# Performance work log

Hardware: AMD Instinct MI355X
Metric: run time of the kernel (lower is better)

The kernel has to match this reference:

```python
import jax, jax.numpy as jnp
import numpy as np

B = 4_194_304
N_LAYERS = 2


def setup_inputs() -> dict:
    key = jax.random.key(0)
    k1, k2 = jax.random.split(key)
    x = jax.random.normal(k1, (B, 2), dtype=jnp.float32)
    q_weights = 0.01 * jax.random.normal(k2, (N_LAYERS, 2), dtype=jnp.float32)
    return {"x": x, "q_weights": q_weights}


def _apply_rx(state, theta, qubit):
    """Apply RX(theta) to `qubit` of a batched 2-qubit state [B,2,2].
    RX(t) = [[cos(t/2), -i sin(t/2)], [-i sin(t/2), cos(t/2)]].
    theta: [B] (per-sample) or scalar (shared weight)."""
    b = state.shape[0]
    theta = jnp.broadcast_to(theta, (b,))
    c = jnp.cos(0.5 * theta)[:, None].astype(state.dtype)
    s = (-1j * jnp.sin(0.5 * theta))[:, None].astype(state.dtype)
    if qubit == 0:
        a0, a1 = state[:, 0, :], state[:, 1, :]
        return jnp.stack([c * a0 + s * a1, s * a0 + c * a1], axis=1)
    else:
        a0, a1 = state[:, :, 0], state[:, :, 1]
        return jnp.stack([c * a0 + s * a1, s * a0 + c * a1], axis=2)


def _cnot01(state):
    # control = qubit0, target = qubit1: swap target amps where control == 1
    return jnp.stack([state[:, 0, :], state[:, 1, ::-1]], axis=1)


def reference(x, q_weights):
    b = x.shape[0]
    # |00> initial state, batched: [B, 2, 2] (axes = qubit0, qubit1)
    state = jnp.zeros((b, 2, 2), dtype=jnp.complex64).at[:, 0, 0].set(1.0)
    # AngleEmbedding (default rotation = RX) with per-sample angles
    state = _apply_rx(state, x[:, 0], 0)
    state = _apply_rx(state, x[:, 1], 1)
    # BasicEntanglerLayers: per layer RX on each wire, then single CNOT(0,1)
    for l in range(q_weights.shape[0]):
        state = _apply_rx(state, q_weights[l, 0], 0)
        state = _apply_rx(state, q_weights[l, 1], 1)
        state = _cnot01(state)
    # <Z_0> = P(qubit0=0) - P(qubit0=1)
    probs = jnp.real(state * jnp.conj(state))
    expz0 = jnp.sum(probs[:, 0, :], axis=-1) - jnp.sum(probs[:, 1, :], axis=-1)
    return (0.5 * (expz0 + 1.0)).astype(jnp.float32).reshape(-1, 1)
```

## Files before the change

kernel.cpp:

```cpp
#include <hip/hip_runtime.h>
#include <math.h>

#define N_LAYERS 2

__device__ __forceinline__ void rx_pair(float2& a, float2& b, float c, float s) {
    float2 na = make_float2(fmaf(c, a.x,  s * b.y), fmaf(c, a.y, -s * b.x));
    float2 nb = make_float2(fmaf(s, a.y,  c * b.x), fmaf(-s, a.x, c * b.y));
    a = na; b = nb;
}

__global__ void qnet_precompute_K(const float* __restrict__ w, float* __restrict__ K) {
    if (threadIdx.x != 0 || blockIdx.x != 0) return;

    float2 U[4][4];
    for (int j = 0; j < 4; ++j)
        for (int r = 0; r < 4; ++r)
            U[j][r] = make_float2(j == r ? 1.f : 0.f, 0.f);

    for (int l = 0; l < N_LAYERS; ++l) {
        float t0 = 0.5f * w[2 * l + 0];
        float t1 = 0.5f * w[2 * l + 1];
        float c0 = cosf(t0), s0 = sinf(t0);
        float c1 = cosf(t1), s1 = sinf(t1);
        for (int j = 0; j < 4; ++j) {
            rx_pair(U[j][0], U[j][2], c0, s0);
            rx_pair(U[j][1], U[j][3], c0, s0);
            rx_pair(U[j][0], U[j][1], c1, s1);
            rx_pair(U[j][2], U[j][3], c1, s1);
            float2 tmp = U[j][2]; U[j][2] = U[j][3]; U[j][3] = tmp;
        }
    }

    float Mre[4][4], Mim[4][4];
    for (int j = 0; j < 4; ++j)
        for (int k = 0; k < 4; ++k) {
            float re = 0.f, im = 0.f;
            for (int m = 0; m < 2; ++m) {
                re += U[j][m].x * U[k][m].x + U[j][m].y * U[k][m].y;
                im += U[j][m].x * U[k][m].y - U[j][m].y * U[k][m].x;
            }
            Mre[j][k] = re; Mim[j][k] = im;
        }

    float N00 = Mre[0][0], N11 = Mre[1][1], N22 = Mre[2][2], N33 = Mre[3][3];
    float N01 = Mim[0][1];
    float N23 = Mim[2][3];
    float N02 = Mim[0][2];
    float N13 = Mim[1][3];
    float N03 = -Mre[0][3];
    float N12 = Mre[1][2];

    K[0] = 0.25f * (N00 + N11 + N22 + N33);
    K[1] = 0.25f * (N00 - N11 + N22 - N33);
    K[2] = 0.50f * (N01 + N23);
    K[3] = 0.25f * (N00 + N11 - N22 - N33);
    K[4] = 0.25f * (N00 - N11 - N22 + N33);
    K[5] = 0.50f * (N01 - N23);
    K[6] = 0.50f * (N02 + N13);
    K[7] = 0.50f * (N02 - N13);
    K[8] = 0.50f * (N03 + N12);
}

__device__ __forceinline__ float qnet_eval1(float x0, float x1,
                                            float k0, float k1, float k2,
                                            float k3, float k4, float k5,
                                            float k6, float k7, float k8) {
    float X0 = __cosf(x0), S0 = __sinf(x0);
    float X1 = __cosf(x1), S1 = __sinf(x1);
    float t0 = fmaf(k2, S1, fmaf(k1, X1, k0));
    float t1 = fmaf(k5, S1, fmaf(k4, X1, k3));
    float t2 = fmaf(k8, S1, fmaf(k7, X1, k6));
    return fmaf(S0, t2, fmaf(X0, t1, t0));
}

__global__ __launch_bounds__(256) void qnet_eval_kernel(
    const float4* __restrict__ x, const float* __restrict__ K,
    float2* __restrict__ out, int n2) {
    int i = blockIdx.x * blockDim.x + threadIdx.x;
    float k0 = K[0], k1 = K[1], k2 = K[2];
    float k3 = K[3], k4 = K[4], k5 = K[5];
    float k6 = K[6], k7 = K[7], k8 = K[8];
    if (i >= n2) return;
    float4 xv = x[i];
    float r0 = qnet_eval1(xv.x, xv.y, k0, k1, k2, k3, k4, k5, k6, k7, k8);
    float r1 = qnet_eval1(xv.z, xv.w, k0, k1, k2, k3, k4, k5, k6, k7, k8);
    out[i] = make_float2(r0, r1);
}

extern "C" void kernel_launch(void* const* d_in, const int* in_sizes, int n_in,
                              void* d_out, int out_size, void* d_ws, size_t ws_size,
                              hipStream_t stream) {
    const float* x = (const float*)d_in[0];
    const float* w = (const float*)d_in[1];
    float* K = (float*)d_ws;
    float* out = (float*)d_out;

    qnet_precompute_K<<<1, 64, 0, stream>>>(w, K);

    int n2 = in_sizes[0] / 4;
    int blocks = (n2 + 255) / 256;
    qnet_eval_kernel<<<blocks, 256, 0, stream>>>(
        (const float4*)x, K, (float2*)out, n2);
}
```

Measured before the change: 79.97 us.

## Fuse K precompute into eval kernel with 4 samples per thread and nontemporal stores

Removes the separate single-thread precompute launch by having thread 0 of every block compute the nine coefficients into shared memory, with input loads issued before the barrier so they overlap that work. Each thread now handles four samples, using two float4 loads and one nontemporal 16-byte store. This drops one kernel launch and its serialization, but every block repeats the small trig and matrix computation serially behind a __syncthreads, and the precompute switches to fast __cosf/__sinf. The tail is fine because the size is divisible by 8.

```diff
diff --git a/kernel.cpp b/kernel.cpp
--- a/kernel.cpp
+++ b/kernel.cpp
@@ -2,6 +2,8 @@
 #include <math.h>
 
 #define N_LAYERS 2
+
+typedef float vfloat4 __attribute__((ext_vector_type(4)));
 
 __device__ __forceinline__ void rx_pair(float2& a, float2& b, float c, float s) {
     float2 na = make_float2(fmaf(c, a.x,  s * b.y), fmaf(c, a.y, -s * b.x));
@@ -9,9 +11,7 @@
     a = na; b = nb;
 }
 
-__global__ void qnet_precompute_K(const float* __restrict__ w, float* __restrict__ K) {
-    if (threadIdx.x != 0 || blockIdx.x != 0) return;
-
+__device__ void compute_K(const float* __restrict__ w, float* __restrict__ K) {
     float2 U[4][4];
     for (int j = 0; j < 4; ++j)
         for (int r = 0; r < 4; ++r)
@@ -20,8 +20,8 @@
     for (int l = 0; l < N_LAYERS; ++l) {
         float t0 = 0.5f * w[2 * l + 0];
         float t1 = 0.5f * w[2 * l + 1];
-        float c0 = cosf(t0), s0 = sinf(t0);
-        float c1 = cosf(t1), s1 = sinf(t1);
+        float c0 = __cosf(t0), s0 = __sinf(t0);
+        float c1 = __cosf(t1), s1 = __sinf(t1);
         for (int j = 0; j < 4; ++j) {
             rx_pair(U[j][0], U[j][2], c0, s0);
             rx_pair(U[j][1], U[j][3], c0, s0);
@@ -43,12 +43,8 @@
         }
 
     float N00 = Mre[0][0], N11 = Mre[1][1], N22 = Mre[2][2], N33 = Mre[3][3];
-    float N01 = Mim[0][1];
-    float N23 = Mim[2][3];
-    float N02 = Mim[0][2];
-    float N13 = Mim[1][3];
-    float N03 = -Mre[0][3];
-    float N12 = Mre[1][2];
+    float N01 = Mim[0][1], N23 = Mim[2][3], N02 = Mim[0][2], N13 = Mim[1][3];
+    float N03 = -Mre[0][3], N12 = Mre[1][2];
 
     K[0] = 0.25f * (N00 + N11 + N22 + N33);
     K[1] = 0.25f * (N00 - N11 + N22 - N33);
@@ -73,18 +69,34 @@
     return fmaf(S0, t2, fmaf(X0, t1, t0));
 }
 
-__global__ __launch_bounds__(256) void qnet_eval_kernel(
-    const float4* __restrict__ x, const float* __restrict__ K,
-    float2* __restrict__ out, int n2) {
+__global__ __launch_bounds__(256) void qnet_fused_kernel(
+    const float4* __restrict__ x, const float* __restrict__ w,
+    vfloat4* __restrict__ out, int nthreads) {
     int i = blockIdx.x * blockDim.x + threadIdx.x;
-    float k0 = K[0], k1 = K[1], k2 = K[2];
-    float k3 = K[3], k4 = K[4], k5 = K[5];
-    float k6 = K[6], k7 = K[7], k8 = K[8];
-    if (i >= n2) return;
-    float4 xv = x[i];
-    float r0 = qnet_eval1(xv.x, xv.y, k0, k1, k2, k3, k4, k5, k6, k7, k8);
-    float r1 = qnet_eval1(xv.z, xv.w, k0, k1, k2, k3, k4, k5, k6, k7, k8);
-    out[i] = make_float2(r0, r1);
+    bool act = (i < nthreads);
+
+    float4 xa, xb;
+    if (act) {
+        xa = x[2 * i + 0];
+        xb = x[2 * i + 1];
+    }
+
+    __shared__ float Ks[9];
+    if (threadIdx.x == 0) compute_K(w, Ks);
+    __syncthreads();
+
+    float k0 = Ks[0], k1 = Ks[1], k2 = Ks[2];
+    float k3 = Ks[3], k4 = Ks[4], k5 = Ks[5];
+    float k6 = Ks[6], k7 = Ks[7], k8 = Ks[8];
+
+    if (act) {
+        vfloat4 r;
+        r.x = qnet_eval1(xa.x, xa.y, k0, k1, k2, k3, k4, k5, k6, k7, k8);
+        r.y = qnet_eval1(xa.z, xa.w, k0, k1, k2, k3, k4, k5, k6, k7, k8);
+        r.z = qnet_eval1(xb.x, xb.y, k0, k1, k2, k3, k4, k5, k6, k7, k8);
+        r.w = qnet_eval1(xb.z, xb.w, k0, k1, k2, k3, k4, k5, k6, k7, k8);
+        __builtin_nontemporal_store(r, &out[i]);
+    }
 }
 
 extern "C" void kernel_launch(void* const* d_in, const int* in_sizes, int n_in,
@@ -92,13 +104,9 @@
                               hipStream_t stream) {
     const float* x = (const float*)d_in[0];
     const float* w = (const float*)d_in[1];
-    float* K = (float*)d_ws;
-    float* out = (float*)d_out;
 
-    qnet_precompute_K<<<1, 64, 0, stream>>>(w, K);
-
-    int n2 = in_sizes[0] / 4;
-    int blocks = (n2 + 255) / 256;
-    qnet_eval_kernel<<<blocks, 256, 0, stream>>>(
-        (const float4*)x, K, (float2*)out, n2);
+    int nthreads = in_sizes[0] / 8;
+    int blocks = (nthreads + 255) / 256;
+    qnet_fused_kernel<<<blocks, 256, 0, stream>>>(
+        (const float4*)x, w, (vfloat4*)d_out, nthreads);
 }
```

Result: faster. 77.29 us (-3.4%).
